# Optimization experiments

Measured on AMD Instinct MI355X. Metric: run time of the kernel, lower is better.

## Reference

```python
import jax, jax.numpy as jnp
import numpy as np
from jax.ops import segment_sum, segment_max

N_GENE, D_IN, HID, HEADS = 100000, 128, 128, 4
N_DRUG, N_DIS = 10000, 5000


def gcn_conv(x, src, dst, W, b, n):
    # PyG GCNConv: add self loops, symmetric deg^-1/2 normalization, scatter-add
    h = x @ W  # [n, hid]
    loop = jnp.arange(n)
    s = jnp.concatenate([src, loop])
    d = jnp.concatenate([dst, loop])
    deg = segment_sum(jnp.ones(d.shape[0], h.dtype), d, num_segments=n)
    dis = jnp.where(deg > 0, jax.lax.rsqrt(deg), 0.0)
    norm = dis[s] * dis[d]  # [E+n]
    return segment_sum(h[s] * norm[:, None], d, num_segments=n) + b


def gat_conv(xs, xd, src, dst, W, att_s, att_d, b, n_dst, heads=HEADS):
    # PyG GATConv (bipartite, shared lin, add_self_loops=False, concat=False)
    C = W.shape[1] // heads
    hs = (xs @ W).reshape(-1, heads, C)  # [Ns,H,C]
    hd = (xd @ W).reshape(-1, heads, C)  # [Nd,H,C]
    a_s = (hs * att_s).sum(-1)  # [Ns,H]
    a_d = (hd * att_d).sum(-1)  # [Nd,H]
    e = jax.nn.leaky_relu(a_s[src] + a_d[dst], 0.2)  # [E,H]
    m = segment_max(e, dst, num_segments=n_dst)
    m = jnp.where(jnp.isfinite(m), m, 0.0)
    ex = jnp.exp(e - m[dst])
    denom = segment_sum(ex, dst, num_segments=n_dst)
    alpha = ex / (denom[dst] + 1e-16)  # per-dst softmax
    out = segment_sum(hs[src] * alpha[:, :, None], dst, num_segments=n_dst)  # [Nd,H,C]
    return out.mean(axis=1) + b


def setup_inputs() -> dict:
    key = jax.random.key(0)
    ks = jax.random.split(key, 24)
    Eg, Ed, Ec = 1000000, 250000, 250000
    sc = 1.0 / np.sqrt(HID)
    inp = {
        'gene_nodes': jax.random.normal(ks[0], (N_GENE, D_IN), jnp.float32),
        'drug_edges': jnp.stack([jax.random.randint(ks[1], (Ed,), 0, N_DRUG),
                                 jax.random.randint(ks[2], (Ed,), 0, N_GENE)]),
        'disease_edges': jnp.stack([jax.random.randint(ks[3], (Ec,), 0, N_DIS),
                                    jax.random.randint(ks[4], (Ec,), 0, N_GENE)]),
        'gene_edges': jax.random.randint(ks[5], (2, Eg), 0, N_GENE),
        'gcn1_w': jax.random.normal(ks[6], (D_IN, HID), jnp.float32) * sc,
        'gcn1_b': jnp.zeros((HID,), jnp.float32),
        'gcn2_w': jax.random.normal(ks[7], (HID, HID), jnp.float32) * sc,
        'gcn2_b': jnp.zeros((HID,), jnp.float32),
        'drug_embed': jax.random.normal(ks[8], (N_DRUG, HID), jnp.float32),
        'disease_embed': jax.random.normal(ks[9], (N_DIS, HID), jnp.float32),
        'gat_d_w': jax.random.normal(ks[10], (HID, HEADS * HID), jnp.float32) * sc,
        'gat_d_att_src': jax.random.normal(ks[11], (HEADS, HID), jnp.float32) * sc,
        'gat_d_att_dst': jax.random.normal(ks[12], (HEADS, HID), jnp.float32) * sc,
        'gat_d_b': jnp.zeros((HID,), jnp.float32),
        'gat_c_w': jax.random.normal(ks[13], (HID, HEADS * HID), jnp.float32) * sc,
        'gat_c_att_src': jax.random.normal(ks[14], (HEADS, HID), jnp.float32) * sc,
        'gat_c_att_dst': jax.random.normal(ks[15], (HEADS, HID), jnp.float32) * sc,
        'gat_c_b': jnp.zeros((HID,), jnp.float32),
        'fuse_w': jax.random.normal(ks[16], (3 * HID, HID), jnp.float32) * sc,
        'fuse_b': jnp.zeros((HID,), jnp.float32),
    }
    return inp


def reference(gene_nodes, drug_edges, disease_edges, gene_edges,
              gcn1_w, gcn1_b, gcn2_w, gcn2_b, drug_embed, disease_embed,
              gat_d_w, gat_d_att_src, gat_d_att_dst, gat_d_b,
              gat_c_w, gat_c_att_src, gat_c_att_dst, gat_c_b,
              fuse_w, fuse_b):
    gs, gd = gene_edges[0], gene_edges[1]
    x = jax.nn.relu(gcn_conv(gene_nodes, gs, gd, gcn1_w, gcn1_b, N_GENE))
    x = jax.nn.relu(gcn_conv(x, gs, gd, gcn2_w, gcn2_b, N_GENE))
    # hetero GAT: drug->gene and disease->gene, HeteroConv aggr='mean'
    g_drug = gat_conv(drug_embed, x, drug_edges[0], drug_edges[1],
                      gat_d_w, gat_d_att_src, gat_d_att_dst, gat_d_b, N_GENE)
    g_dis = gat_conv(disease_embed, x, disease_edges[0], disease_edges[1],
                     gat_c_w, gat_c_att_src, gat_c_att_dst, gat_c_b, N_GENE)
    gene_out = 0.5 * (g_drug + g_dis)
    bg = gene_out.mean(axis=0, keepdims=True)   # [1,HID]
    bd = drug_embed.mean(axis=0, keepdims=True)
    bc = disease_embed.mean(axis=0, keepdims=True)
    return jnp.concatenate([bg, bd, bc], axis=-1) @ fuse_w + fuse_b  # [1,HID]
```

## Files before the change

### kernel.cpp

```cpp
#include <hip/hip_runtime.h>
#include <hip/hip_fp16.h>

#define NG 100000
#define NDR 10000
#define NDI 5000
#define NDOM (3 * NG + NDR + NDI)
#define NBUCK 616
#define BCHUNK 4096
#define EPT 16

typedef _Float16 f16x8 __attribute__((ext_vector_type(8)));
typedef float f32x4 __attribute__((ext_vector_type(4)));

__device__ __forceinline__ void atomAddF(float* p, float v) { unsafeAtomicAdd(p, v); }

static inline int cdiv_h(int a, int b) { return (a + b - 1) / b; }

__device__ __host__ __forceinline__ int bcap(int b) {
  return b < 586 ? 8192 : (b < 606 ? 24576 : 32768);
}
__device__ __host__ __forceinline__ int bbase(int b) {
  if (b < 586) return b * 8192;
  if (b < 606) return 586 * 8192 + (b - 586) * 24576;
  return 586 * 8192 + 20 * 24576 + (b - 606) * 32768;
}
#define NPAIR (586 * 8192 + 20 * 24576 + 10 * 32768)

__device__ __forceinline__ void prep_body(int blk,
                                          const float* W1, const float* W2,
                                          const float* Wd, const float* Wc,
                                          const float* attd_d, const float* attd_c,
                                          __half* Wt1, __half* Wt2,
                                          __half* Wtd, __half* Wtc, float* watt) {
  if (blk == 10) {
    int t = threadIdx.x;
    for (int slot = t; slot < 1024; slot += 256) {
      int i = slot >> 3, s8 = slot & 7;
      const float* W = (s8 < 4) ? Wd : Wc;
      const float* A = (s8 < 4) ? attd_d : attd_c;
      int h = s8 & 3;
      float s = 0.f;
      for (int cc = 0; cc < 128; cc++) s += W[(size_t)i * 512 + h * 128 + cc] * A[h * 128 + cc];
      watt[i * 8 + s8] = s;
    }
    return;
  }
  const float* W;
  __half* Wt;
  int N, base;
  if (blk == 0) { W = W1; Wt = Wt1; N = 128; base = 0; }
  else if (blk == 1) { W = W2; Wt = Wt2; N = 128; base = 0; }
  else if (blk < 6) { W = Wd; Wt = Wtd; N = 512; base = (blk - 2) * 16384; }
  else { W = Wc; Wt = Wtc; N = 512; base = (blk - 6) * 16384; }
  for (int q = threadIdx.x; q < 16384; q += 256) {
    int qq = base + q;
    int n = qq >> 7, k = qq & 127;
    Wt[qq] = __float2half(W[(size_t)k * N + n]);
  }
}

__global__ __launch_bounds__(256) void k_front(const float* __restrict__ W1,
                                               const float* __restrict__ W2,
                                               const float* __restrict__ Wd,
                                               const float* __restrict__ Wc,
                                               const float* __restrict__ attd_d,
                                               const float* __restrict__ attd_c,
                                               __half* __restrict__ Wt1,
                                               __half* __restrict__ Wt2,
                                               __half* __restrict__ Wtd,
                                               __half* __restrict__ Wtc,
                                               float* __restrict__ watt,
                                               int* __restrict__ cursor616) {
  if (blockIdx.x == 11) {
    for (int i = threadIdx.x; i < NBUCK; i += 256) cursor616[i] = bbase(i);
    return;
  }
  prep_body(blockIdx.x, W1, W2, Wd, Wc, attd_d, attd_c, Wt1, Wt2, Wtd, Wtc, watt);
}

__device__ __forceinline__ void decode(int idx, const int* __restrict__ ge, int Eg_,
                                       const int* __restrict__ de, int Ed_,
                                       const int* __restrict__ ce, int Ec_,
                                       unsigned& node, unsigned& val) {
  int B1 = Eg_, B2 = Eg_ + Ed_, B3 = Eg_ + 2 * Ed_, B4 = B3 + Ec_;
  if (idx < B1) { node = (unsigned)ge[Eg_ + idx]; val = (unsigned)ge[idx]; }
  else if (idx < B2) { int i = idx - B1; node = NG + (unsigned)de[Ed_ + i]; val = (unsigned)de[i]; }
  else if (idx < B3) { int i = idx - B2; node = 3 * NG + (unsigned)de[i]; val = (unsigned)de[Ed_ + i]; }
  else if (idx < B4) { int i = idx - B3; node = 2 * NG + (unsigned)ce[Ec_ + i]; val = (unsigned)ce[i]; }
  else { int i = idx - B4; node = 3 * NG + NDR + (unsigned)ce[i]; val = (unsigned)ce[Ec_ + i]; }
}

__global__ __launch_bounds__(256) void k_binH(const int* __restrict__ ge, int Eg_,
                                              const int* __restrict__ de, int Ed_,
                                              const int* __restrict__ ce, int Ec_,
                                              int* __restrict__ cursor616,
                                              unsigned* __restrict__ pairs) {
  __shared__ int hist[NBUCK];
  int t = threadIdx.x;
  for (int i = t; i < NBUCK; i += 256) hist[i] = 0;
  __syncthreads();
  const int ME = Eg_ + 2 * (Ed_ + Ec_);
  int base = blockIdx.x * BCHUNK;
  int cnt = min(BCHUNK, ME - base);

  unsigned nodeR[EPT], valR[EPT];
#pragma unroll
  for (int k = 0; k < EPT; k++) {
    int j = t + k * 256;
    nodeR[k] = 0xFFFFFFFFu;
    if (j < cnt) decode(base + j, ge, Eg_, de, Ed_, ce, Ec_, nodeR[k], valR[k]);
  }
#pragma unroll
  for (int k = 0; k < EPT; k++)
    if (nodeR[k] != 0xFFFFFFFFu) atomicAdd(&hist[nodeR[k] >> 9], 1);
  __syncthreads();
  for (int b = t; b < NBUCK; b += 256) {
    int h = hist[b];
    hist[b] = h ? atomicAdd(&cursor616[b], h) : 0;
  }
  __syncthreads();
#pragma unroll
  for (int k = 0; k < EPT; k++) {
    if (nodeR[k] == 0xFFFFFFFFu) continue;
    unsigned b = nodeR[k] >> 9;
    int p = atomicAdd(&hist[b], 1);
    if (p < bbase(b) + bcap(b))
      pairs[p] = ((nodeR[k] - (b << 9)) << 17) | valR[k];
  }
}

__global__ __launch_bounds__(256) void k_scan616(const int* __restrict__ cursor616,
                                                 int* __restrict__ bucketbase) {
  __shared__ int s[256];
  int t = threadIdx.x;
  int loc[3];
  int sum = 0;
#pragma unroll
  for (int k = 0; k < 3; k++) {
    int b = 3 * t + k;
    int v = (b < NBUCK) ? min(cursor616[b] - bbase(b), bcap(b)) : 0;
    loc[k] = sum;
    sum += v;
  }
  s[t] = sum;
  __syncthreads();
  for (int off = 1; off < 256; off <<= 1) {
    int add = (t >= off) ? s[t - off] : 0;
    __syncthreads();
    s[t] += add;
    __syncthreads();
  }
  int excl = s[t] - sum;
#pragma unroll
  for (int k = 0; k < 3; k++) {
    int b = 3 * t + k;
    if (b < NBUCK) bucketbase[b] = excl + loc[k];
  }
}

__global__ __launch_bounds__(256) void k_placeAll(const int* __restrict__ cursor616,
                                                  const int* __restrict__ bucketbase,
                                                  const unsigned* __restrict__ pairs,
                                                  int* __restrict__ rowptr,
                                                  float* __restrict__ dis,
                                                  int* __restrict__ adj) {
  __shared__ int hist[512];
  __shared__ int scan[256];
  int b = blockIdx.x;
  int n0 = b << 9;
  int n1 = min(n0 + 512, NDOM);
  int t = threadIdx.x;
  hist[t] = 0;
  hist[t + 256] = 0;
  __syncthreads();
  int base = bbase(b);
  int cnt = min(cursor616[b] - base, bcap(b));
  for (int i = base + t; i < base + cnt; i += 256) atomicAdd(&hist[pairs[i] >> 17], 1);
  __syncthreads();
  int h0 = hist[2 * t], h1 = hist[2 * t + 1];
  int sum = h0 + h1;
  scan[t] = sum;
  __syncthreads();
  for (int off = 1; off < 256; off <<= 1) {
    int add = (t >= off) ? scan[t - off] : 0;
    __syncthreads();
    scan[t] += add;
    __syncthreads();
  }
  int excl = scan[t] - sum;
  int bb = bucketbase[b];
  int i0 = 2 * t, i1 = 2 * t + 1;
  int r0 = bb + excl, r1 = bb + excl + h0;
  if (n0 + i0 < n1) {
    rowptr[n0 + i0] = r0;
    if (n0 + i0 < NG) dis[n0 + i0] = rsqrtf((float)h0 + 1.0f);
  }
  if (n0 + i1 < n1) {
    rowptr[n0 + i1] = r1;
    if (n0 + i1 < NG) dis[n0 + i1] = rsqrtf((float)h1 + 1.0f);
    if (n0 + i1 == NDOM - 1) rowptr[NDOM] = r1 + h1;
  }
  if (n0 + i0 == NDOM - 1) rowptr[NDOM] = r0 + h0;
  __syncthreads();
  hist[i0] = r0;
  hist[i1] = r1;
  __syncthreads();
  for (int i = base + t; i < base + cnt; i += 256) {
    unsigned pr = pairs[i];
    int p = atomicAdd(&hist[pr >> 17], 1);
    adj[p] = (int)(pr & 0x1FFFFu);
  }
}

template <int INF16>
__global__ __launch_bounds__(256) void k_mgemm(const void* __restrict__ Xv,
                                               const __half* __restrict__ Wt, int M,
                                               const float* __restrict__ dis,
                                               __half* __restrict__ hh) {
  __shared__ __align__(16) char lds[48 * 1024];
  char* As = lds;
  char* Bs = lds + 16 * 1024;
  const int t = threadIdx.x;
  const int row0 = blockIdx.x * 64;

#pragma unroll
  for (int rep = 0; rep < 8; rep++) {
    int q = t + rep * 256;
    int r = q >> 4, c16 = (q & 15) * 16;
    uint4 v = *(const uint4*)((const char*)Wt + r * 256 + c16);
    *(uint4*)(Bs + ((r * 256 + c16) ^ ((r & 7) << 4))) = v;
  }
  if (INF16 == 0) {
    const float* X = (const float*)Xv;
#pragma unroll
    for (int rep = 0; rep < 8; rep++) {
      int q = t + rep * 256;
      int r = q >> 5, c4 = (q & 31) * 4;
      int gr = row0 + r;
      float4 xv = make_float4(0.f, 0.f, 0.f, 0.f);
      if (gr < M) xv = *(const float4*)&X[(size_t)gr * 128 + c4];
      __half2 h0 = __floats2half2_rn(xv.x, xv.y);
      __half2 h1 = __floats2half2_rn(xv.z, xv.w);
      uint2 pk;
      pk.x = *(unsigned*)&h0;
      pk.y = *(unsigned*)&h1;
      *(uint2*)(As + ((r * 256 + c4 * 2) ^ ((r & 7) << 4))) = pk;
    }
  } else {
    const __half* X = (const __half*)Xv;
#pragma unroll
    for (int rep = 0; rep < 4; rep++) {
      int q = t + rep * 256;
      int r = q >> 4, c16 = (q & 15) * 16;
      int gr = row0 + r;
      uint4 v = make_uint4(0u, 0u, 0u, 0u);
      if (gr < M) v = *(const uint4*)((const char*)X + (size_t)gr * 256 + c16);
      *(uint4*)(As + ((r * 256 + c16) ^ ((r & 7) << 4))) = v;
    }
  }
  __syncthreads();

  const int w = t >> 6, l = t & 63;
  const int lr = l & 15, lk = l >> 4;
  f32x4 acc[8] = {};
#pragma unroll
  for (int s = 0; s < 4; s++) {
    int arow = w * 16 + lr;
    f16x8 a = *(const f16x8*)(As + ((arow * 256 + lk * 16 + s * 64) ^ ((arow & 7) << 4)));
#pragma unroll
    for (int nt = 0; nt < 8; nt++) {
      int brow = nt * 16 + lr;
      f16x8 b = *(const f16x8*)(Bs + ((brow * 256 + lk * 16 + s * 64) ^ ((brow & 7) << 4)));
      acc[nt] = __builtin_amdgcn_mfma_f32_16x16x32_f16(a, b, acc[nt], 0, 0, 0);
    }
  }
  float ddv[4];
  int rowb = row0 + w * 16 + lk * 4;
#pragma unroll
  for (int j = 0; j < 4; j++) ddv[j] = (rowb + j < M) ? dis[rowb + j] : 0.f;
#pragma unroll
  for (int nt = 0; nt < 8; nt++) {
#pragma unroll
    for (int j = 0; j < 4; j++) {
      int row = rowb + j;
      if (row < M) hh[(size_t)row * 128 + nt * 16 + lr] = __float2half(acc[nt][j] * ddv[j]);
    }
  }
}

__global__ __launch_bounds__(256) void k_mgat(const float* __restrict__ Xd,
                                              const float* __restrict__ Xc,
                                              const __half* __restrict__ Wtd,
                                              const __half* __restrict__ Wtc,
                                              const float* __restrict__ attSd,
                                              const float* __restrict__ attSc,
                                              __half* __restrict__ hsd,
                                              __half* __restrict__ hsc,
                                              float* __restrict__ a_s_d,
                                              float* __restrict__ a_s_c) {
  __shared__ __align__(16) char lds[48 * 1024];
  char* As = lds;
  char* Bs = lds + 16 * 1024;
  const int t = threadIdx.x;
  const int nbd = (NDR + 63) >> 6;
  const int q = blockIdx.x >= nbd;
  const int bx = q ? blockIdx.x - nbd : blockIdx.x;
  const int M = q ? NDI : NDR;
  const float* X = q ? Xc : Xd;
  const __half* Wt = q ? Wtc : Wtd;
  const float* attS = q ? attSc : attSd;
  __half* hs = q ? hsc : hsd;
  float* a_s = q ? a_s_c : a_s_d;
  const int row0 = bx * 64;
  const int h = blockIdx.y;
  const __half* Wth = Wt + (size_t)h * 128 * 128;

#pragma unroll
  for (int rep = 0; rep < 8; rep++) {
    int r = (t + rep * 256) >> 4, c16 = ((t + rep * 256) & 15) * 16;
    uint4 v = *(const uint4*)((const char*)Wth + r * 256 + c16);
    *(uint4*)(Bs + ((r * 256 + c16) ^ ((r & 7) << 4))) = v;
  }
#pragma unroll
  for (int rep = 0; rep < 8; rep++) {
    int qq = t + rep * 256;
    int r = qq >> 5, c4 = (qq & 31) * 4;
    int gr = row0 + r;
    float4 xv = make_float4(0.f, 0.f, 0.f, 0.f);
    if (gr < M) xv = *(const float4*)&X[(size_t)gr * 128 + c4];
    __half2 h0 = __floats2half2_rn(xv.x, xv.y);
    __half2 h1 = __floats2half2_rn(xv.z, xv.w);
    uint2 pk;
    pk.x = *(unsigned*)&h0;
    pk.y = *(unsigned*)&h1;
    *(uint2*)(As + ((r * 256 + c4 * 2) ^ ((r & 7) << 4))) = pk;
  }
  __syncthreads();

  const int w = t >> 6, l = t & 63;
  const int lr = l & 15, lk = l >> 4;
  f32x4 acc[8] = {};
#pragma unroll
  for (int s = 0; s < 4; s++) {
    int arow = w * 16 + lr;
    f16x8 a = *(const f16x8*)(As + ((arow * 256 + lk * 16 + s * 64) ^ ((arow & 7) << 4)));
#pragma unroll
    for (int nt = 0; nt < 8; nt++) {
      int brow = nt * 16 + lr;
      f16x8 b = *(const f16x8*)(Bs + ((brow * 256 + lk * 16 + s * 64) ^ ((brow & 7) << 4)));
      acc[nt] = __builtin_amdgcn_mfma_f32_16x16x32_f16(a, b, acc[nt], 0, 0, 0);
    }
  }
  float av[8];
#pragma unroll
  for (int nt = 0; nt < 8; nt++) av[nt] = attS[h * 128 + nt * 16 + lr];

  int rowb = row0 + w * 16 + lk * 4;
  float p[4] = {0.f, 0.f, 0.f, 0.f};
#pragma unroll
  for (int nt = 0; nt < 8; nt++) {
#pragma unroll
    for (int j = 0; j < 4; j++) {
      int row = rowb + j;
      if (row < M) hs[(size_t)row * 512 + h * 128 + nt * 16 + lr] = __float2half(acc[nt][j]);
      p[j] += acc[nt][j] * av[nt];
    }
  }
#pragma unroll
  for (int m = 1; m < 16; m <<= 1) {
#pragma unroll
    for (int j = 0; j < 4; j++) p[j] += __shfl_xor(p[j], m);
  }
  if (lr == 0) {
#pragma unroll
    for (int j = 0; j < 4; j++) {
      int row = rowb + j;
      if (row < M) a_s[(size_t)row * 4 + h] = p[j];
    }
  }
}

template <int FIN>
__global__ __launch_bounds__(256) void k_gather(const __half* __restrict__ hh,
                                                const int* __restrict__ rowptr,
                                                const int* __restrict__ adj,
                                                const float* __restrict__ dis,
                                                const float* __restrict__ b,
                                                const float* __restrict__ watt,
                                                void* __restrict__ outv, int n) {
  int wid = threadIdx.x >> 6;
  int lane = threadIdx.x & 63;
  int d0 = blockIdx.x * 8 + wid * 2;
  if (d0 >= n) return;
  int d1 = d0 + 1;
  bool hasB = (d1 < n);
  int p0a = rowptr[d0], p1a = rowptr[d0 + 1];
  int p0b = p1a, p1b = hasB ? rowptr[d1 + 1] : p1a;
  int c = lane * 2;
  float2 sA, sB = make_float2(0.f, 0.f);
  {
    unsigned v = *(const unsigned*)&hh[(size_t)d0 * 128 + c];
    sA = __half22float2(*(__half2*)&v);
  }
  if (hasB) {
    unsigned v = *(const unsigned*)&hh[(size_t)d1 * 128 + c];
    sB = __half22float2(*(__half2*)&v);
  }
  int mA = p1a - p0a, mB = p1b - p0b;
  if (mA <= 64 && mB <= 64) {
    int idxA = (lane < mA) ? adj[p0a + lane] : 0;
    int idxB = (lane < mB) ? adj[p0b + lane] : 0;
    int M = mA > mB ? mA : mB;
    for (int j = 0; j < M; j += 4) {
      int nb[8];
      bool ok[8];
#pragma unroll
      for (int u = 0; u < 4; u++) {
        int ja = j + u;
        int va = __shfl(idxA, ja & 63);
        ok[u] = ja < mA;
        nb[u] = ok[u] ? va : d0;
        int vb = __shfl(idxB, ja & 63);
        ok[4 + u] = ja < mB;
        nb[4 + u] = ok[4 + u] ? vb : d0;
      }
      unsigned v[8];
#pragma unroll
      for (int u = 0; u < 8; u++) v[u] = *(const unsigned*)&hh[(size_t)nb[u] * 128 + c];
#pragma unroll
      for (int u = 0; u < 4; u++) {
        float2 f = __half22float2(*(__half2*)&v[u]);
        if (ok[u]) { sA.x += f.x; sA.y += f.y; }
      }
#pragma unroll
      for (int u = 4; u < 8; u++) {
        float2 f = __half22float2(*(__half2*)&v[u]);
        if (ok[u]) { sB.x += f.x; sB.y += f.y; }
      }
    }
  } else {
    for (int base = p0a; base < p1a; base += 64) {
      int m = min(p1a - base, 64);
      int idx = (lane < m) ? adj[base + lane] : 0;
      for (int j = 0; j < m; j++) {
        int nb = __shfl(idx, j);
        unsigned v = *(const unsigned*)&hh[(size_t)nb * 128 + c];
        float2 f = __half22float2(*(__half2*)&v);
        sA.x += f.x;
        sA.y += f.y;
      }
    }
    for (int base = p0b; base < p1b; base += 64) {
      int m = min(p1b - base, 64);
      int idx = (lane < m) ? adj[base + lane] : 0;
      for (int j = 0; j < m; j++) {
        int nb = __shfl(idx, j);
        unsigned v = *(const unsigned*)&hh[(size_t)nb * 128 + c];
        float2 f = __half22float2(*(__half2*)&v);
        sB.x += f.x;
        sB.y += f.y;
      }
    }
  }
  float ddA = dis[d0];
  float ddB = hasB ? dis[d1] : 0.f;
  float bc0 = b[c], bc1 = b[c + 1];
  float xA0 = fmaxf(ddA * sA.x + bc0, 0.f);
  float xA1 = fmaxf(ddA * sA.y + bc1, 0.f);
  float xB0 = fmaxf(ddB * sB.x + bc0, 0.f);
  float xB1 = fmaxf(ddB * sB.y + bc1, 0.f);
  if (FIN == 1) {
    __half* o = (__half*)outv;
    __half2 hA = __floats2half2_rn(xA0, xA1);
    *(__half2*)&o[(size_t)d0 * 128 + c] = hA;
    if (hasB) {
      __half2 hB = __floats2half2_rn(xB0, xB1);
      *(__half2*)&o[(size_t)d1 * 128 + c] = hB;
    }
  } else {
    float* o = (float*)outv;
    float pA[8], pB[8];
    const float* w0 = &watt[c * 8];
#pragma unroll
    for (int h = 0; h < 8; h++) {
      pA[h] = xA0 * w0[h] + xA1 * w0[8 + h];
      pB[h] = xB0 * w0[h] + xB1 * w0[8 + h];
    }
#pragma unroll
    for (int mm = 32; mm; mm >>= 1) {
#pragma unroll
      for (int h = 0; h < 8; h++) {
        pA[h] += __shfl_xor(pA[h], mm);
        pB[h] += __shfl_xor(pB[h], mm);
      }
    }
    if (lane == 0) {
      *(float4*)&o[(size_t)d0 * 8] = make_float4(pA[0], pA[1], pA[2], pA[3]);
      *(float4*)&o[(size_t)d0 * 8 + 4] = make_float4(pA[4], pA[5], pA[6], pA[7]);
      if (hasB) {
        *(float4*)&o[(size_t)d1 * 8] = make_float4(pB[0], pB[1], pB[2], pB[3]);
        *(float4*)&o[(size_t)d1 * 8 + 4] = make_float4(pB[4], pB[5], pB[6], pB[7]);
      }
    }
  }
}

__global__ __launch_bounds__(256) void k_edgeA(const int* __restrict__ rowptr,
                                               const int* __restrict__ adj,
                                               const float* __restrict__ a_s_d,
                                               const float* __restrict__ a_s_c,
                                               const float* __restrict__ att,
                                               float* __restrict__ denom_d,
                                               float* __restrict__ denom_c) {
  int nb1 = (NG + 255) >> 8;
  int blk = blockIdx.x;
  int q = blk >= nb1;
  int d = (blk - (q ? nb1 : 0)) * 256 + threadIdx.x;
  if (d >= NG) return;
  const int* rp = rowptr + NG + (q ? NG : 0);
  const float* a_s = q ? a_s_c : a_s_d;
  float* den = q ? denom_c : denom_d;
  int p0 = rp[d], p1 = rp[d + 1];
  float4 ad4 = *(const float4*)&att[(size_t)d * 8 + q * 4];
  float4 acc = make_float4(0.f, 0.f, 0.f, 0.f);
  for (int p = p0; p < p1; p++) {
    int s = adj[p];
    float4 as4 = *(const float4*)&a_s[(size_t)s * 4];
    float v0 = as4.x + ad4.x, v1 = as4.y + ad4.y, v2 = as4.z + ad4.z, v3 = as4.w + ad4.w;
    v0 = v0 > 0.f ? v0 : 0.2f * v0;
    v1 = v1 > 0.f ? v1 : 0.2f * v1;
    v2 = v2 > 0.f ? v2 : 0.2f * v2;
    v3 = v3 > 0.f ? v3 : 0.2f * v3;
    acc.x += __expf(fminf(v0, 50.f));
    acc.y += __expf(fminf(v1, 50.f));
    acc.z += __expf(fminf(v2, 50.f));
    acc.w += __expf(fminf(v3, 50.f));
  }
  *(float4*)&den[(size_t)d * 4] = acc;
}

__global__ __launch_bounds__(256) void k_edgeB(const int* __restrict__ rowptr,
                                               const int* __restrict__ adj,
                                               const float* __restrict__ a_s_d,
                                               const float* __restrict__ a_s_c,
                                               const float* __restrict__ att,
                                               const float* __restrict__ denom_d,
                                               const float* __restrict__ denom_c,
                                               float* __restrict__ wsrc_d,
                                               float* __restrict__ wsrc_c) {
  int gw = (blockIdx.x * 256 + threadIdx.x) >> 6;
  int lane = threadIdx.x & 63;
  int q = gw >= NDR;
  int s = q ? gw - NDR : gw;
  if (q && s >= NDI) return;
  const int* rp = rowptr + 3 * NG + (q ? NDR : 0);
  const float* a_s = q ? a_s_c : a_s_d;
  const float* den = q ? denom_c : denom_d;
  float* ws = q ? wsrc_c : wsrc_d;
  int p0 = rp[s], p1 = rp[s + 1];
  float4 as4 = *(const float4*)&a_s[(size_t)s * 4];
  int attoff = q * 4;
  float4 acc = make_float4(0.f, 0.f, 0.f, 0.f);
  for (int p = p0 + lane; p < p1; p += 64) {
    int d = adj[p];
    float4 ad4 = *(const float4*)&att[(size_t)d * 8 + attoff];
    float4 dn = *(const float4*)&den[(size_t)d * 4];
    float v0 = as4.x + ad4.x, v1 = as4.y + ad4.y, v2 = as4.z + ad4.z, v3 = as4.w + ad4.w;
    v0 = v0 > 0.f ? v0 : 0.2f * v0;
    v1 = v1 > 0.f ? v1 : 0.2f * v1;
    v2 = v2 > 0.f ? v2 : 0.2f * v2;
    v3 = v3 > 0.f ? v3 : 0.2f * v3;
    acc.x += __expf(fminf(v0, 50.f)) / (dn.x + 1e-16f);
    acc.y += __expf(fminf(v1, 50.f)) / (dn.y + 1e-16f);
    acc.z += __expf(fminf(v2, 50.f)) / (dn.z + 1e-16f);
    acc.w += __expf(fminf(v3, 50.f)) / (dn.w + 1e-16f);
  }
#pragma unroll
  for (int m = 1; m < 64; m <<= 1) {
    acc.x += __shfl_xor(acc.x, m);
    acc.y += __shfl_xor(acc.y, m);
    acc.z += __shfl_xor(acc.z, m);
    acc.w += __shfl_xor(acc.w, m);
  }
  if (lane == 0) *(float4*)&ws[(size_t)s * 4] = acc;
}

__global__ __launch_bounds__(512) void k_sum(const __half* __restrict__ hs_d,
                                             const float* __restrict__ wsrc_d,
                                             float* __restrict__ S_d,
                                             const __half* __restrict__ hs_c,
                                             const float* __restrict__ wsrc_c,
                                             float* __restrict__ S_c,
                                             const float* __restrict__ xd,
                                             float* __restrict__ od,
                                             const float* __restrict__ xc,
                                             float* __restrict__ oc) {
  int t = threadIdx.x;
  const int nws_d = (NDR + 63) >> 6;
  const int nws_c = (NDI + 63) >> 6;
  const int ncs_d = (NDR + 511) >> 9;
  int blk = blockIdx.x;
  if (blk < nws_d + nws_c) {
    int q = blk >= nws_d;
    const __half* hs = q ? hs_c : hs_d;
    const float* wsrc = q ? wsrc_c : wsrc_d;
    float* S = q ? S_c : S_d;
    int N = q ? NDI : NDR;
    int r0 = (q ? blk - nws_d : blk) * 64;
    int h = t >> 7;
    int r1 = min(r0 + 64, N);
    float acc = 0.f;
    for (int r = r0; r < r1; r++) acc += wsrc[r * 4 + h] * __half2float(hs[(size_t)r * 512 + t]);
    atomAddF(&S[t], acc);
  } else {
    int cb = blk - nws_d - nws_c;
    int q = cb >= ncs_d;
    const float* x = q ? xc : xd;
    float* o = q ? oc : od;
    int N = q ? NDI : NDR;
    int r0 = (q ? cb - ncs_d : cb) * 512 + (t >> 7) * 128;
    int col = t & 127;
    int r1 = min(r0 + 128, N);
    float acc = 0.f;
    for (int r = r0; r < r1; r++) acc += x[(size_t)r * 128 + col];
    if (r0 < N) atomAddF(&o[col], acc);
  }
}

__global__ __launch_bounds__(128) void k_final(const float* __restrict__ S_d,
                                               const float* __restrict__ S_c,
                                               const float* __restrict__ bdsum,
                                               const float* __restrict__ bcsum,
                                               const float* __restrict__ bd_bias,
                                               const float* __restrict__ bc_bias,
                                               const float* __restrict__ fuse_w,
                                               const float* __restrict__ fuse_b,
                                               float* __restrict__ out) {
  __shared__ float cat[384];
  int t = threadIdx.x;
  float sd = S_d[t] + S_d[128 + t] + S_d[256 + t] + S_d[384 + t];
  float sc = S_c[t] + S_c[128 + t] + S_c[256 + t] + S_c[384 + t];
  const float inv = 1.0f / (4.0f * (float)NG);
  cat[t] = 0.5f * (sd * inv + bd_bias[t] + sc * inv + bc_bias[t]);
  cat[128 + t] = bdsum[t] * (1.0f / (float)NDR);
  cat[256 + t] = bcsum[t] * (1.0f / (float)NDI);
  __syncthreads();
  float o = fuse_b[t];
  for (int k = 0; k < 384; k++) o += cat[k] * fuse_w[k * 128 + t];
  out[t] = o;
}

extern "C" void kernel_launch(void* const* d_in, const int* in_sizes, int n_in,
                              void* d_out, int out_size, void* d_ws, size_t ws_size,
                              hipStream_t stream) {
  const float* gene_nodes   = (const float*)d_in[0];
  const int*   drug_edges   = (const int*)d_in[1];
  const int*   dise_edges   = (const int*)d_in[2];
  const int*   gene_edges   = (const int*)d_in[3];
  const float* gcn1_w       = (const float*)d_in[4];
  const float* gcn1_b       = (const float*)d_in[5];
  const float* gcn2_w       = (const float*)d_in[6];
  const float* gcn2_b       = (const float*)d_in[7];
  const float* drug_embed   = (const float*)d_in[8];
  const float* dise_embed   = (const float*)d_in[9];
  const float* gat_d_w      = (const float*)d_in[10];
  const float* gat_d_att_s  = (const float*)d_in[11];
  const float* gat_d_att_d  = (const float*)d_in[12];
  const float* gat_d_b      = (const float*)d_in[13];
  const float* gat_c_w      = (const float*)d_in[14];
  const float* gat_c_att_s  = (const float*)d_in[15];
  const float* gat_c_att_d  = (const float*)d_in[16];
  const float* gat_c_b      = (const float*)d_in[17];
  const float* fuse_w       = (const float*)d_in[18];
  const float* fuse_b       = (const float*)d_in[19];
  const int Ed = in_sizes[1] / 2;
  const int Ec = in_sizes[2] / 2;
  const int Eg = in_sizes[3] / 2;
  float* out = (float*)d_out;
  (void)n_in; (void)out_size; (void)ws_size;

  const int ME = Eg + 2 * (Ed + Ec);

  char* w = (char*)d_ws;
  auto alloc = [&](size_t n) {
    char* p = w;
    w += (n + 511) & ~(size_t)511;
    return p;
  };
  char* z0 = w;
  float* S_d        = (float*)alloc(512 * 4);
  float* S_c        = (float*)alloc(512 * 4);
  float* bdsum      = (float*)alloc(512);
  float* bcsum      = (float*)alloc(512);
  size_t zbytes = (size_t)(w - z0);
  float* denom_d    = (float*)alloc((size_t)NG * 16);
  float* denom_c    = (float*)alloc((size_t)NG * 16);
  float* wsrc_d     = (float*)alloc((size_t)NDR * 16);
  float* wsrc_c     = (float*)alloc((size_t)NDI * 16);
  float* dis        = (float*)alloc((size_t)NG * 4);
  float* watt       = (float*)alloc(128 * 8 * 4);
  float* att        = (float*)alloc((size_t)NG * 8 * 4);
  float* a_s_d      = (float*)alloc((size_t)NDR * 16);
  float* a_s_c      = (float*)alloc((size_t)NDI * 16);
  int* rowptr       = (int*)alloc((size_t)(NDOM + 1) * 4);
  int* cursor616    = (int*)alloc((size_t)NBUCK * 4);
  int* bucketbase   = (int*)alloc((size_t)(NBUCK + 1) * 4);
  int* adj          = (int*)alloc((size_t)ME * 4);
  unsigned* pairs   = (unsigned*)alloc((size_t)NPAIR * 4);
  __half* Wt1       = (__half*)alloc((size_t)128 * 128 * 2);
  __half* Wt2       = (__half*)alloc((size_t)128 * 128 * 2);
  __half* Wtd       = (__half*)alloc((size_t)512 * 128 * 2);
  __half* Wtc       = (__half*)alloc((size_t)512 * 128 * 2);
  __half* hh        = (__half*)alloc((size_t)NG * 128 * 2);
  __half* x1        = (__half*)alloc((size_t)NG * 128 * 2);
  __half* hs_d      = (__half*)alloc((size_t)NDR * 512 * 2);
  __half* hs_c      = (__half*)alloc((size_t)NDI * 512 * 2);

  hipMemsetAsync(z0, 0, zbytes, stream);

  k_front<<<12, 256, 0, stream>>>(gcn1_w, gcn2_w, gat_d_w, gat_c_w, gat_d_att_d, gat_c_att_d,
                                  Wt1, Wt2, Wtd, Wtc, watt, cursor616);

  k_binH<<<cdiv_h(ME, BCHUNK), 256, 0, stream>>>(gene_edges, Eg, drug_edges, Ed, dise_edges, Ec,
                                                 cursor616, pairs);
  k_scan616<<<1, 256, 0, stream>>>(cursor616, bucketbase);
  k_placeAll<<<NBUCK, 256, 0, stream>>>(cursor616, bucketbase, pairs, rowptr, dis, adj);

  k_mgemm<0><<<cdiv_h(NG, 64), 256, 0, stream>>>(gene_nodes, Wt1, NG, dis, hh);
  k_gather<1><<<cdiv_h(NG, 8), 256, 0, stream>>>(hh, rowptr, adj, dis, gcn1_b, nullptr, x1, NG);

  k_mgemm<1><<<cdiv_h(NG, 64), 256, 0, stream>>>(x1, Wt2, NG, dis, hh);
  k_gather<2><<<cdiv_h(NG, 8), 256, 0, stream>>>(hh, rowptr, adj, dis, gcn2_b, watt, att, NG);

  k_mgat<<<dim3(cdiv_h(NDR, 64) + cdiv_h(NDI, 64), 4), 256, 0, stream>>>(
      drug_embed, dise_embed, Wtd, Wtc, gat_d_att_s, gat_c_att_s, hs_d, hs_c, a_s_d, a_s_c);

  k_edgeA<<<2 * cdiv_h(NG, 256), 256, 0, stream>>>(rowptr, adj, a_s_d, a_s_c, att, denom_d, denom_c);
  k_edgeB<<<cdiv_h((NDR + NDI) * 64, 256), 256, 0, stream>>>(rowptr, adj, a_s_d, a_s_c, att,
                                                             denom_d, denom_c, wsrc_d, wsrc_c);

  int nsum = (cdiv_h(NDR, 64) + cdiv_h(NDI, 64)) + (cdiv_h(NDR, 512) + cdiv_h(NDI, 512));
  k_sum<<<nsum, 512, 0, stream>>>(hs_d, wsrc_d, S_d, hs_c, wsrc_c, S_c,
                                  drug_embed, bdsum, dise_embed, bcsum);

  k_final<<<1, 128, 0, stream>>>(S_d, S_c, bdsum, bcsum, gat_d_b, gat_c_b, fuse_w, fuse_b, out);
}
```

Before: 361.4 us.

## Fuse GAT projection into first GEMM and GAT denominators into second gather

Merges several launches. The GAT source projection blocks now run in the same grid as the first gene GEMM. The per-destination softmax denominator pass moves into the second GCN gather, with half a wave per edge type. The drug and disease column sums move into the front prep kernel. The gather now uses one wave per node with 8-way unrolled loads instead of two nodes per wave, which removes the extra launches and one pass over rowptr/adj/att, at the cost of heavier gather blocks and possible imbalance.

```diff
diff --git a/kernel.cpp b/kernel.cpp
--- a/kernel.cpp
+++ b/kernel.cpp
@@ -70,12 +70,31 @@
                                                __half* __restrict__ Wtd,
                                                __half* __restrict__ Wtc,
                                                float* __restrict__ watt,
-                                               int* __restrict__ cursor616) {
-  if (blockIdx.x == 11) {
+                                               int* __restrict__ cursor616,
+                                               const float* __restrict__ xd,
+                                               float* __restrict__ od,
+                                               const float* __restrict__ xc,
+                                               float* __restrict__ oc) {
+  int blk = blockIdx.x;
+  if (blk < 11) {
+    prep_body(blk, W1, W2, Wd, Wc, attd_d, attd_c, Wt1, Wt2, Wtd, Wtc, watt);
+    return;
+  }
+  if (blk == 11) {
     for (int i = threadIdx.x; i < NBUCK; i += 256) cursor616[i] = bbase(i);
     return;
   }
-  prep_body(blockIdx.x, W1, W2, Wd, Wc, attd_d, attd_c, Wt1, Wt2, Wtd, Wtc, watt);
+  int cb = blk - 12;
+  int q = cb >= 20;
+  const float* x = q ? xc : xd;
+  float* o = q ? oc : od;
+  int N = q ? NDI : NDR;
+  int r0 = (q ? cb - 20 : cb) * 512 + (int)(threadIdx.x >> 7) * 256;
+  int col = threadIdx.x & 127;
+  int r1 = min(r0 + 256, N);
+  float acc = 0.f;
+  for (int r = r0; r < r1; r++) acc += x[(size_t)r * 128 + col];
+  if (r0 < N) atomAddF(&o[col], acc);
 }
 
 __device__ __forceinline__ void decode(int idx, const int* __restrict__ ge, int Eg_,
@@ -213,15 +232,14 @@
 }
 
 template <int INF16>
-__global__ __launch_bounds__(256) void k_mgemm(const void* __restrict__ Xv,
-                                               const __half* __restrict__ Wt, int M,
-                                               const float* __restrict__ dis,
-                                               __half* __restrict__ hh) {
-  __shared__ __align__(16) char lds[48 * 1024];
+__device__ __forceinline__ void mgemm_body(char* lds, int bx, const void* __restrict__ Xv,
+                                           const __half* __restrict__ Wt, int M,
+                                           const float* __restrict__ dis,
+                                           __half* __restrict__ hh) {
   char* As = lds;
   char* Bs = lds + 16 * 1024;
   const int t = threadIdx.x;
-  const int row0 = blockIdx.x * 64;
+  const int row0 = bx * 64;
 
 #pragma unroll
   for (int rep = 0; rep < 8; rep++) {
@@ -288,23 +306,23 @@
   }
 }
 
-__global__ __launch_bounds__(256) void k_mgat(const float* __restrict__ Xd,
-                                              const float* __restrict__ Xc,
-                                              const __half* __restrict__ Wtd,
-                                              const __half* __restrict__ Wtc,
-                                              const float* __restrict__ attSd,
-                                              const float* __restrict__ attSc,
-                                              __half* __restrict__ hsd,
-                                              __half* __restrict__ hsc,
-                                              float* __restrict__ a_s_d,
-                                              float* __restrict__ a_s_c) {
-  __shared__ __align__(16) char lds[48 * 1024];
+__device__ __forceinline__ void mgat_body(char* lds, int bxx, int h,
+                                          const float* __restrict__ Xd,
+                                          const float* __restrict__ Xc,
+                                          const __half* __restrict__ Wtd,
+                                          const __half* __restrict__ Wtc,
+                                          const float* __restrict__ attSd,
+                                          const float* __restrict__ attSc,
+                                          __half* __restrict__ hsd,
+                                          __half* __restrict__ hsc,
+                                          float* __restrict__ a_s_d,
+                                          float* __restrict__ a_s_c) {
   char* As = lds;
   char* Bs = lds + 16 * 1024;
   const int t = threadIdx.x;
   const int nbd = (NDR + 63) >> 6;
-  const int q = blockIdx.x >= nbd;
-  const int bx = q ? blockIdx.x - nbd : blockIdx.x;
+  const int q = bxx >= nbd;
+  const int bx = q ? bxx - nbd : bxx;
   const int M = q ? NDI : NDR;
   const float* X = q ? Xc : Xd;
   const __half* Wt = q ? Wtc : Wtd;
@@ -312,7 +330,6 @@
   __half* hs = q ? hsc : hsd;
   float* a_s = q ? a_s_c : a_s_d;
   const int row0 = bx * 64;
-  const int h = blockIdx.y;
   const __half* Wth = Wt + (size_t)h * 128 * 128;
 
 #pragma unroll
@@ -380,6 +397,39 @@
   }
 }
 
+__global__ __launch_bounds__(256) void k_mm1(const float* __restrict__ X1,
+                                             const __half* __restrict__ Wt1,
+                                             const float* __restrict__ dis,
+                                             __half* __restrict__ hh,
+                                             const float* __restrict__ Xd,
+                                             const float* __restrict__ Xc,
+                                             const __half* __restrict__ Wtd,
+                                             const __half* __restrict__ Wtc,
+                                             const float* __restrict__ attSd,
+                                             const float* __restrict__ attSc,
+                                             __half* __restrict__ hsd,
+                                             __half* __restrict__ hsc,
+                                             float* __restrict__ a_s_d,
+                                             float* __restrict__ a_s_c) {
+  __shared__ __align__(16) char lds[48 * 1024];
+  const int NB1 = (NG + 63) >> 6;
+  if ((int)blockIdx.x < NB1) {
+    mgemm_body<0>(lds, blockIdx.x, X1, Wt1, NG, dis, hh);
+    return;
+  }
+  int r = blockIdx.x - NB1;
+  mgat_body(lds, r >> 2, r & 3, Xd, Xc, Wtd, Wtc, attSd, attSc, hsd, hsc, a_s_d, a_s_c);
+}
+
+template <int INF16>
+__global__ __launch_bounds__(256) void k_mgemm(const void* __restrict__ Xv,
+                                               const __half* __restrict__ Wt, int M,
+                                               const float* __restrict__ dis,
+                                               __half* __restrict__ hh) {
+  __shared__ __align__(16) char lds[48 * 1024];
+  mgemm_body<INF16>(lds, blockIdx.x, Xv, Wt, M, dis, hh);
+}
+
 template <int FIN>
 __global__ __launch_bounds__(256) void k_gather(const __half* __restrict__ hh,
                                                 const int* __restrict__ rowptr,
@@ -387,156 +437,114 @@
                                                 const float* __restrict__ dis,
                                                 const float* __restrict__ b,
                                                 const float* __restrict__ watt,
-                                                void* __restrict__ outv, int n) {
+                                                void* __restrict__ outv, int n,
+                                                const float* __restrict__ a_s_d,
+                                                const float* __restrict__ a_s_c,
+                                                float* __restrict__ denom_d,
+                                                float* __restrict__ denom_c) {
   int wid = threadIdx.x >> 6;
   int lane = threadIdx.x & 63;
-  int d0 = blockIdx.x * 8 + wid * 2;
-  if (d0 >= n) return;
-  int d1 = d0 + 1;
-  bool hasB = (d1 < n);
-  int p0a = rowptr[d0], p1a = rowptr[d0 + 1];
-  int p0b = p1a, p1b = hasB ? rowptr[d1 + 1] : p1a;
+  int d = blockIdx.x * 4 + wid;
+  if (d >= n) return;
+  int p0 = rowptr[d], p1 = rowptr[d + 1];
   int c = lane * 2;
-  float2 sA, sB = make_float2(0.f, 0.f);
+  float2 s;
   {
-    unsigned v = *(const unsigned*)&hh[(size_t)d0 * 128 + c];
-    sA = __half22float2(*(__half2*)&v);
-  }
-  if (hasB) {
-    unsigned v = *(const unsigned*)&hh[(size_t)d1 * 128 + c];
-    sB = __half22float2(*(__half2*)&v);
-  }
-  int mA = p1a - p0a, mB = p1b - p0b;
-  if (mA <= 64 && mB <= 64) {
-    int idxA = (lane < mA) ? adj[p0a + lane] : 0;
-    int idxB = (lane < mB) ? adj[p0b + lane] : 0;
-    int M = mA > mB ? mA : mB;
-    for (int j = 0; j < M; j += 4) {
+    unsigned v = *(const unsigned*)&hh[(size_t)d * 128 + c];
+    s = __half22float2(*(__half2*)&v);
+  }
+  for (int base = p0; base < p1; base += 64) {
+    int remain = p1 - base;
+    int m = remain < 64 ? remain : 64;
+    int idx = (lane < m) ? adj[base + lane] : 0;
+    int j = 0;
+    for (; j + 8 <= m; j += 8) {
       int nb[8];
-      bool ok[8];
-#pragma unroll
-      for (int u = 0; u < 4; u++) {
-        int ja = j + u;
-        int va = __shfl(idxA, ja & 63);
-        ok[u] = ja < mA;
-        nb[u] = ok[u] ? va : d0;
-        int vb = __shfl(idxB, ja & 63);
-        ok[4 + u] = ja < mB;
-        nb[4 + u] = ok[4 + u] ? vb : d0;
+      unsigned v[8];
+#pragma unroll
+      for (int u = 0; u < 8; u++) nb[u] = __shfl(idx, j + u);
+#pragma unroll
+      for (int u = 0; u < 8; u++) v[u] = *(const unsigned*)&hh[(size_t)nb[u] * 128 + c];
+#pragma unroll
+      for (int u = 0; u < 8; u++) {
+        float2 f = __half22float2(*(__half2*)&v[u]);
+        s.x += f.x;
+        s.y += f.y;
       }
-      unsigned v[8];
-#pragma unroll
-      for (int u = 0; u < 8; u++) v[u] = *(const unsigned*)&hh[(size_t)nb[u] * 128 + c];
+    }
+    for (; j + 4 <= m; j += 4) {
+      int nb[4];
+      unsigned v[4];
+#pragma unroll
+      for (int u = 0; u < 4; u++) nb[u] = __shfl(idx, j + u);
+#pragma unroll
+      for (int u = 0; u < 4; u++) v[u] = *(const unsigned*)&hh[(size_t)nb[u] * 128 + c];
 #pragma unroll
       for (int u = 0; u < 4; u++) {
         float2 f = __half22float2(*(__half2*)&v[u]);
-        if (ok[u]) { sA.x += f.x; sA.y += f.y; }
+        s.x += f.x;
+        s.y += f.y;
       }
-#pragma unroll
-      for (int u = 4; u < 8; u++) {
-        float2 f = __half22float2(*(__half2*)&v[u]);
-        if (ok[u]) { sB.x += f.x; sB.y += f.y; }
-      }
-    }
-  } else {
-    for (int base = p0a; base < p1a; base += 64) {
-      int m = min(p1a - base, 64);
-      int idx = (lane < m) ? adj[base + lane] : 0;
-      for (int j = 0; j < m; j++) {
-        int nb = __shfl(idx, j);
-        unsigned v = *(const unsigned*)&hh[(size_t)nb * 128 + c];
-        float2 f = __half22float2(*(__half2*)&v);
-        sA.x += f.x;
-        sA.y += f.y;
-      }
-    }
-    for (int base = p0b; base < p1b; base += 64) {
-      int m = min(p1b - base, 64);
-      int idx = (lane < m) ? adj[base + lane] : 0;
-      for (int j = 0; j < m; j++) {
-        int nb = __shfl(idx, j);
-        unsigned v = *(const unsigned*)&hh[(size_t)nb * 128 + c];
-        float2 f = __half22float2(*(__half2*)&v);
-        sB.x += f.x;
-        sB.y += f.y;
-      }
-    }
-  }
-  float ddA = dis[d0];
-  float ddB = hasB ? dis[d1] : 0.f;
-  float bc0 = b[c], bc1 = b[c + 1];
-  float xA0 = fmaxf(ddA * sA.x + bc0, 0.f);
-  float xA1 = fmaxf(ddA * sA.y + bc1, 0.f);
-  float xB0 = fmaxf(ddB * sB.x + bc0, 0.f);
-  float xB1 = fmaxf(ddB * sB.y + bc1, 0.f);
+    }
+    for (; j < m; j++) {
+      int nb = __shfl(idx, j);
+      unsigned v = *(const unsigned*)&hh[(size_t)nb * 128 + c];
+      float2 f = __half22float2(*(__half2*)&v);
+      s.x += f.x;
+      s.y += f.y;
+    }
+  }
+  float dd = dis[d];
+  float x0 = fmaxf(dd * s.x + b[c], 0.f);
+  float x1v = fmaxf(dd * s.y + b[c + 1], 0.f);
   if (FIN == 1) {
     __half* o = (__half*)outv;
-    __half2 hA = __floats2half2_rn(xA0, xA1);
-    *(__half2*)&o[(size_t)d0 * 128 + c] = hA;
-    if (hasB) {
-      __half2 hB = __floats2half2_rn(xB0, xB1);
-      *(__half2*)&o[(size_t)d1 * 128 + c] = hB;
-    }
+    __half2 hv = __floats2half2_rn(x0, x1v);
+    *(__half2*)&o[(size_t)d * 128 + c] = hv;
   } else {
-    float* o = (float*)outv;
-    float pA[8], pB[8];
+    float p[8];
     const float* w0 = &watt[c * 8];
 #pragma unroll
-    for (int h = 0; h < 8; h++) {
-      pA[h] = xA0 * w0[h] + xA1 * w0[8 + h];
-      pB[h] = xB0 * w0[h] + xB1 * w0[8 + h];
-    }
+    for (int h = 0; h < 8; h++) p[h] = x0 * w0[h] + x1v * w0[8 + h];
 #pragma unroll
     for (int mm = 32; mm; mm >>= 1) {
 #pragma unroll
-      for (int h = 0; h < 8; h++) {
-        pA[h] += __shfl_xor(pA[h], mm);
-        pB[h] += __shfl_xor(pB[h], mm);
-      }
-    }
+      for (int h = 0; h < 8; h++) p[h] += __shfl_xor(p[h], mm);
+    }
+    float* attp = (float*)outv;
     if (lane == 0) {
-      *(float4*)&o[(size_t)d0 * 8] = make_float4(pA[0], pA[1], pA[2], pA[3]);
-      *(float4*)&o[(size_t)d0 * 8 + 4] = make_float4(pA[4], pA[5], pA[6], pA[7]);
-      if (hasB) {
-        *(float4*)&o[(size_t)d1 * 8] = make_float4(pB[0], pB[1], pB[2], pB[3]);
-        *(float4*)&o[(size_t)d1 * 8 + 4] = make_float4(pB[4], pB[5], pB[6], pB[7]);
-      }
-    }
-  }
-}
-
-__global__ __launch_bounds__(256) void k_edgeA(const int* __restrict__ rowptr,
-                                               const int* __restrict__ adj,
-                                               const float* __restrict__ a_s_d,
-                                               const float* __restrict__ a_s_c,
-                                               const float* __restrict__ att,
-                                               float* __restrict__ denom_d,
-                                               float* __restrict__ denom_c) {
-  int nb1 = (NG + 255) >> 8;
-  int blk = blockIdx.x;
-  int q = blk >= nb1;
-  int d = (blk - (q ? nb1 : 0)) * 256 + threadIdx.x;
-  if (d >= NG) return;
-  const int* rp = rowptr + NG + (q ? NG : 0);
-  const float* a_s = q ? a_s_c : a_s_d;
-  float* den = q ? denom_c : denom_d;
-  int p0 = rp[d], p1 = rp[d + 1];
-  float4 ad4 = *(const float4*)&att[(size_t)d * 8 + q * 4];
-  float4 acc = make_float4(0.f, 0.f, 0.f, 0.f);
-  for (int p = p0; p < p1; p++) {
-    int s = adj[p];
-    float4 as4 = *(const float4*)&a_s[(size_t)s * 4];
-    float v0 = as4.x + ad4.x, v1 = as4.y + ad4.y, v2 = as4.z + ad4.z, v3 = as4.w + ad4.w;
-    v0 = v0 > 0.f ? v0 : 0.2f * v0;
-    v1 = v1 > 0.f ? v1 : 0.2f * v1;
-    v2 = v2 > 0.f ? v2 : 0.2f * v2;
-    v3 = v3 > 0.f ? v3 : 0.2f * v3;
-    acc.x += __expf(fminf(v0, 50.f));
-    acc.y += __expf(fminf(v1, 50.f));
-    acc.z += __expf(fminf(v2, 50.f));
-    acc.w += __expf(fminf(v3, 50.f));
-  }
-  *(float4*)&den[(size_t)d * 4] = acc;
+      *(float4*)&attp[(size_t)d * 8] = make_float4(p[0], p[1], p[2], p[3]);
+      *(float4*)&attp[(size_t)d * 8 + 4] = make_float4(p[4], p[5], p[6], p[7]);
+    }
+    int half = lane >> 5, sl = lane & 31;
+    const int* rp = rowptr + NG + half * NG;
+    int q0 = rp[d], q1 = rp[d + 1];
+    const float* a_s = half ? a_s_c : a_s_d;
+    float* den = half ? denom_c : denom_d;
+    float e0 = p[half * 4], e1 = p[half * 4 + 1], e2 = p[half * 4 + 2], e3 = p[half * 4 + 3];
+    float4 acc4 = make_float4(0.f, 0.f, 0.f, 0.f);
+    for (int pp = q0 + sl; pp < q1; pp += 32) {
+      int src = adj[pp];
+      float4 as4 = *(const float4*)&a_s[(size_t)src * 4];
+      float v0 = as4.x + e0, v1 = as4.y + e1, v2 = as4.z + e2, v3 = as4.w + e3;
+      v0 = v0 > 0.f ? v0 : 0.2f * v0;
+      v1 = v1 > 0.f ? v1 : 0.2f * v1;
+      v2 = v2 > 0.f ? v2 : 0.2f * v2;
+      v3 = v3 > 0.f ? v3 : 0.2f * v3;
+      acc4.x += __expf(fminf(v0, 50.f));
+      acc4.y += __expf(fminf(v1, 50.f));
+      acc4.z += __expf(fminf(v2, 50.f));
+      acc4.w += __expf(fminf(v3, 50.f));
+    }
+#pragma unroll
+    for (int mm = 1; mm < 32; mm <<= 1) {
+      acc4.x += __shfl_xor(acc4.x, mm);
+      acc4.y += __shfl_xor(acc4.y, mm);
+      acc4.z += __shfl_xor(acc4.z, mm);
+      acc4.w += __shfl_xor(acc4.w, mm);
+    }
+    if (sl == 0) *(float4*)&den[(size_t)d * 4] = acc4;
+  }
 }
 
 __global__ __launch_bounds__(256) void k_edgeB(const int* __restrict__ rowptr,
@@ -590,41 +598,21 @@
                                              float* __restrict__ S_d,
                                              const __half* __restrict__ hs_c,
                                              const float* __restrict__ wsrc_c,
-                                             float* __restrict__ S_c,
-                                             const float* __restrict__ xd,
-                                             float* __restrict__ od,
-                                             const float* __restrict__ xc,
-                                             float* __restrict__ oc) {
+                                             float* __restrict__ S_c) {
   int t = threadIdx.x;
   const int nws_d = (NDR + 63) >> 6;
-  const int nws_c = (NDI + 63) >> 6;
-  const int ncs_d = (NDR + 511) >> 9;
   int blk = blockIdx.x;
-  if (blk < nws_d + nws_c) {
-    int q = blk >= nws_d;
-    const __half* hs = q ? hs_c : hs_d;
-    const float* wsrc = q ? wsrc_c : wsrc_d;
-    float* S = q ? S_c : S_d;
-    int N = q ? NDI : NDR;
-    int r0 = (q ? blk - nws_d : blk) * 64;
-    int h = t >> 7;
-    int r1 = min(r0 + 64, N);
-    float acc = 0.f;
-    for (int r = r0; r < r1; r++) acc += wsrc[r * 4 + h] * __half2float(hs[(size_t)r * 512 + t]);
-    atomAddF(&S[t], acc);
-  } else {
-    int cb = blk - nws_d - nws_c;
-    int q = cb >= ncs_d;
-    const float* x = q ? xc : xd;
-    float* o = q ? oc : od;
-    int N = q ? NDI : NDR;
-    int r0 = (q ? cb - ncs_d : cb) * 512 + (t >> 7) * 128;
-    int col = t & 127;
-    int r1 = min(r0 + 128, N);
-    float acc = 0.f;
-    for (int r = r0; r < r1; r++) acc += x[(size_t)r * 128 + col];
-    if (r0 < N) atomAddF(&o[col], acc);
-  }
+  int q = blk >= nws_d;
+  const __half* hs = q ? hs_c : hs_d;
+  const float* wsrc = q ? wsrc_c : wsrc_d;
+  float* S = q ? S_c : S_d;
+  int N = q ? NDI : NDR;
+  int r0 = (q ? blk - nws_d : blk) * 64;
+  int h = t >> 7;
+  int r1 = min(r0 + 64, N);
+  float acc = 0.f;
+  for (int r = r0; r < r1; r++) acc += wsrc[r * 4 + h] * __half2float(hs[(size_t)r * 512 + t]);
+  atomAddF(&S[t], acc);
 }
 
 __global__ __launch_bounds__(128) void k_final(const float* __restrict__ S_d,
@@ -718,30 +706,33 @@
 
   hipMemsetAsync(z0, 0, zbytes, stream);
 
-  k_front<<<12, 256, 0, stream>>>(gcn1_w, gcn2_w, gat_d_w, gat_c_w, gat_d_att_d, gat_c_att_d,
-                                  Wt1, Wt2, Wtd, Wtc, watt, cursor616);
+  k_front<<<42, 256, 0, stream>>>(gcn1_w, gcn2_w, gat_d_w, gat_c_w, gat_d_att_d, gat_c_att_d,
+                                  Wt1, Wt2, Wtd, Wtc, watt, cursor616,
+                                  drug_embed, bdsum, dise_embed, bcsum);
 
   k_binH<<<cdiv_h(ME, BCHUNK), 256, 0, stream>>>(gene_edges, Eg, drug_edges, Ed, dise_edges, Ec,
                                                  cursor616, pairs);
   k_scan616<<<1, 256, 0, stream>>>(cursor616, bucketbase);
   k_placeAll<<<NBUCK, 256, 0, stream>>>(cursor616, bucketbase, pairs, rowptr, dis, adj);
 
-  k_mgemm<0><<<cdiv_h(NG, 64), 256, 0, stream>>>(gene_nodes, Wt1, NG, dis, hh);
-  k_gather<1><<<cdiv_h(NG, 8), 256, 0, stream>>>(hh, rowptr, adj, dis, gcn1_b, nullptr, x1, NG);
-
-  k_mgemm<1><<<cdiv_h(NG, 64), 256, 0, stream>>>(x1, Wt2, NG, dis, hh);
-  k_gather<2><<<cdiv_h(NG, 8), 256, 0, stream>>>(hh, rowptr, adj, dis, gcn2_b, watt, att, NG);
-
-  k_mgat<<<dim3(cdiv_h(NDR, 64) + cdiv_h(NDI, 64), 4), 256, 0, stream>>>(
-      drug_embed, dise_embed, Wtd, Wtc, gat_d_att_s, gat_c_att_s, hs_d, hs_c, a_s_d, a_s_c);
-
-  k_edgeA<<<2 * cdiv_h(NG, 256), 256, 0, stream>>>(rowptr, adj, a_s_d, a_s_c, att, denom_d, denom_c);
+  int nb1 = cdiv_h(NG, 64);
+  int nbg = (cdiv_h(NDR, 64) + cdiv_h(NDI, 64)) * 4;
+  k_mm1<<<nb1 + nbg, 256, 0, stream>>>(gene_nodes, Wt1, dis, hh,
+                                       drug_embed, dise_embed, Wtd, Wtc,
+                                       gat_d_att_s, gat_c_att_s, hs_d, hs_c, a_s_d, a_s_c);
+
+  k_gather<1><<<cdiv_h(NG, 4), 256, 0, stream>>>(hh, rowptr, adj, dis, gcn1_b, nullptr, x1, NG,
+                                                 nullptr, nullptr, nullptr, nullptr);
+
+  k_mgemm<1><<<nb1, 256, 0, stream>>>(x1, Wt2, NG, dis, hh);
+  k_gather<2><<<cdiv_h(NG, 4), 256, 0, stream>>>(hh, rowptr, adj, dis, gcn2_b, watt, att, NG,
+                                                 a_s_d, a_s_c, denom_d, denom_c);
+
   k_edgeB<<<cdiv_h((NDR + NDI) * 64, 256), 256, 0, stream>>>(rowptr, adj, a_s_d, a_s_c, att,
                                                              denom_d, denom_c, wsrc_d, wsrc_c);
 
-  int nsum = (cdiv_h(NDR, 64) + cdiv_h(NDI, 64)) + (cdiv_h(NDR, 512) + cdiv_h(NDI, 512));
-  k_sum<<<nsum, 512, 0, stream>>>(hs_d, wsrc_d, S_d, hs_c, wsrc_c, S_c,
-                                  drug_embed, bdsum, dise_embed, bcsum);
+  k_sum<<<cdiv_h(NDR, 64) + cdiv_h(NDI, 64), 512, 0, stream>>>(hs_d, wsrc_d, S_d,
+                                                               hs_c, wsrc_c, S_c);
 
   k_final<<<1, 128, 0, stream>>>(S_d, S_c, bdsum, bcsum, gat_d_b, gat_c_b, fuse_w, fuse_b, out);
 }
```

Measured after the change: 386.3 us. 6.9% more time.
